# Optimization experiments

Hardware: AMD Instinct MI355X
Metric: run time of the kernel (lower is better)

Reference implementation:

```python
import jax, jax.numpy as jnp
import numpy as np

TARGET_SIZE = 1024
SOURCE_SIZE = 1024


def setup_inputs() -> dict:
    key = jax.random.key(0)
    k1, k2, k3, k4 = jax.random.split(key, 4)
    B, T, S = 16, 1024, 1024
    sentence_state = jax.random.normal(k1, (B, T, TARGET_SIZE), dtype=jnp.float32)
    graph_state = jax.random.normal(k2, (B, S, SOURCE_SIZE), dtype=jnp.float32)
    mask = jax.random.bernoulli(k3, 0.5, (B, T, S))  # bool
    # nn.Linear(target_size+source_size, 1, bias=False).weight flattened
    w = jax.random.normal(k4, (TARGET_SIZE + SOURCE_SIZE,), dtype=jnp.float32) * (
        1.0 / np.sqrt(TARGET_SIZE + SOURCE_SIZE)
    )
    return {"sentence_state": sentence_state, "graph_state": graph_state, "mask": mask, "w": w}


def reference(sentence_state, graph_state, mask, w):
    # Linear on concat([tgt, src]) with out_features=1 decomposes into two dot products:
    # score[b,t,s] = sentence[b,t,:] @ w_t + graph[b,s,:] @ w_s
    w_t = w[:TARGET_SIZE]
    w_s = w[TARGET_SIZE:]
    st = jnp.einsum("btd,d->bt", sentence_state, w_t)  # (B, T)
    gs = jnp.einsum("bsd,d->bs", graph_state, w_s)  # (B, S)
    scores = st[:, :, None] + gs[:, None, :]  # (B, T, S)
    attn = jax.nn.softmax(scores, axis=-1)
    attn = attn * (~mask).astype(attn.dtype)
    norm = jnp.sum(attn, axis=-1, keepdims=True) + 1e-12
    return attn / norm
```

## Files before the change

### kernel.cpp

```cpp
#include <hip/hip_runtime.h>


constexpr int Bb = 16;
constexpr int Tt = 1024;
constexpr int Ss = 1024;
constexpr int Dd = 1024;

__global__ void mask_probe_kernel(const unsigned char* __restrict__ m,
                                  int* __restrict__ ws_flag) {
  __shared__ int nz[4];
  const int t = threadIdx.x;
  if (t < 4) nz[t] = 0;
  __syncthreads();
  uchar4 v = reinterpret_cast<const uchar4*>(m)[t];
  if (v.x) atomicOr(&nz[0], 1);
  if (v.y) atomicOr(&nz[1], 1);
  if (v.z) atomicOr(&nz[2], 1);
  if (v.w) atomicOr(&nz[3], 1);
  __syncthreads();
  if (t == 0) {
    int spread = (nz[0] != 0) + (nz[1] != 0) + (nz[2] != 0) + (nz[3] != 0);
    ws_flag[0] = (spread >= 3) ? 0 : 1;
  }
}

__global__ __launch_bounds__(256) void gs_dot_kernel(
    const float* __restrict__ graph, const float* __restrict__ w_full,
    float* __restrict__ gs) {
  const int lane = threadIdx.x & 63;
  const int wv   = threadIdx.x >> 6;
  const long row = (long)blockIdx.x * 4 + wv;
  const float4* r  = reinterpret_cast<const float4*>(graph) + row * (Dd / 4);
  const float4* ws = reinterpret_cast<const float4*>(w_full + 1024);
  float acc = 0.f;
#pragma unroll
  for (int k = 0; k < 4; ++k) {
    float4 a = r[lane + 64 * k];
    float4 b = ws[lane + 64 * k];
    acc = fmaf(a.x, b.x, acc);
    acc = fmaf(a.y, b.y, acc);
    acc = fmaf(a.z, b.z, acc);
    acc = fmaf(a.w, b.w, acc);
  }
#pragma unroll
  for (int off = 32; off; off >>= 1) acc += __shfl_xor(acc, off, 64);
  if (lane == 0) gs[row] = acc;
}

__global__ __launch_bounds__(256) void PointerGenerator_9259949490200_kernel(
    const float* __restrict__ gs, const unsigned char* __restrict__ mask,
    const int* __restrict__ ws_flag, float* __restrict__ out) {
  __shared__ float p_sh[Ss];
  __shared__ float redbuf[8];
  const int tid  = threadIdx.x;
  const int lane = tid & 63;
  const int wv   = tid >> 6;
  const int b    = blockIdx.y;

  float4 g = reinterpret_cast<const float4*>(gs + (long)b * Ss)[tid];
  float m = fmaxf(fmaxf(g.x, g.y), fmaxf(g.z, g.w));
#pragma unroll
  for (int off = 32; off; off >>= 1) m = fmaxf(m, __shfl_xor(m, off, 64));
  if (lane == 0) redbuf[wv] = m;
  __syncthreads();
  m = fmaxf(fmaxf(redbuf[0], redbuf[1]), fmaxf(redbuf[2], redbuf[3]));
  float4 e = make_float4(__expf(g.x - m), __expf(g.y - m),
                         __expf(g.z - m), __expf(g.w - m));
  float zs = e.x + e.y + e.z + e.w;
#pragma unroll
  for (int off = 32; off; off >>= 1) zs += __shfl_xor(zs, off, 64);
  if (lane == 0) redbuf[4 + wv] = zs;
  __syncthreads();
  const float Z    = redbuf[4] + redbuf[5] + redbuf[6] + redbuf[7];
  const float invZ = 1.0f / Z;
  reinterpret_cast<float4*>(p_sh)[tid] =
      make_float4(e.x * invZ, e.y * invZ, e.z * invZ, e.w * invZ);
  __syncthreads();

  const long t    = (long)blockIdx.x * 4 + wv;
  const long row  = (long)b * Tt + t;
  const int  mode = ws_flag[0];

  uchar4 mk[4];
  if (mode == 0) {
    const uchar4* mrow = reinterpret_cast<const uchar4*>(mask + row * Ss);
#pragma unroll
    for (int k = 0; k < 4; ++k) mk[k] = mrow[lane + 64 * k];
  } else {
    const int4* mrow =
        reinterpret_cast<const int4*>(reinterpret_cast<const int*>(mask) + row * Ss);
#pragma unroll
    for (int k = 0; k < 4; ++k) {
      int4 w = mrow[lane + 64 * k];
      mk[k] = make_uchar4((unsigned char)(w.x != 0), (unsigned char)(w.y != 0),
                          (unsigned char)(w.z != 0), (unsigned char)(w.w != 0));
    }
  }

  float4 p[4];
  float sum = 0.f;
#pragma unroll
  for (int k = 0; k < 4; ++k) {
    const int idx = lane + 64 * k;
    p[k] = reinterpret_cast<const float4*>(p_sh)[idx];
    sum += (mk[k].x ? 0.f : p[k].x) + (mk[k].y ? 0.f : p[k].y) +
           (mk[k].z ? 0.f : p[k].z) + (mk[k].w ? 0.f : p[k].w);
  }
#pragma unroll
  for (int off = 32; off; off >>= 1) sum += __shfl_xor(sum, off, 64);
  const float invD = 1.0f / (sum + 1e-12f);
  float4* orow = reinterpret_cast<float4*>(out + row * Ss);
#pragma unroll
  for (int k = 0; k < 4; ++k) {
    const int idx = lane + 64 * k;
    float4 v;
    v.x = mk[k].x ? 0.f : p[k].x * invD;
    v.y = mk[k].y ? 0.f : p[k].y * invD;
    v.z = mk[k].z ? 0.f : p[k].z * invD;
    v.w = mk[k].w ? 0.f : p[k].w * invD;
    orow[idx] = v;
  }
}

extern "C" void kernel_launch(void* const* d_in, const int* in_sizes, int n_in,
                              void* d_out, int out_size, void* d_ws, size_t ws_size,
                              hipStream_t stream) {
  const float* graph        = (const float*)d_in[1];
  const unsigned char* mask = (const unsigned char*)d_in[2];
  const float* w            = (const float*)d_in[3];
  float* out = (float*)d_out;

  int*   ws_flag = (int*)d_ws;
  float* gs      = (float*)((char*)d_ws + 256);

  mask_probe_kernel<<<1, 256, 0, stream>>>(mask, ws_flag);
  gs_dot_kernel<<<(Bb * Ss) / 4, 256, 0, stream>>>(graph, w, gs);
  PointerGenerator_9259949490200_kernel<<<dim3(Tt / 4, Bb), 256, 0, stream>>>(
      gs, mask, ws_flag, out);
}
```

Measured before the change: 42.40 us.

## Precompute per-batch softmax once, process four rows per wave, nontemporal stores

Moves the per-batch softmax over gs out of the main kernel into a separate 16-block kernel that writes normalized probabilities to workspace and also performs the mask-format probe. The main kernel then loads those probabilities once per wave into registers and reuses them across four output rows, cutting the redundant softmax recomputation that every block previously did. Output writes use nontemporal stores to avoid polluting cache. The cost is an extra global round-trip for p, a serial extra launch dependency, and higher register use from holding four rows of masks.

```diff
diff --git a/kernel.cpp b/kernel.cpp
--- a/kernel.cpp
+++ b/kernel.cpp
@@ -6,23 +6,7 @@
 constexpr int Ss = 1024;
 constexpr int Dd = 1024;
 
-__global__ void mask_probe_kernel(const unsigned char* __restrict__ m,
-                                  int* __restrict__ ws_flag) {
-  __shared__ int nz[4];
-  const int t = threadIdx.x;
-  if (t < 4) nz[t] = 0;
-  __syncthreads();
-  uchar4 v = reinterpret_cast<const uchar4*>(m)[t];
-  if (v.x) atomicOr(&nz[0], 1);
-  if (v.y) atomicOr(&nz[1], 1);
-  if (v.z) atomicOr(&nz[2], 1);
-  if (v.w) atomicOr(&nz[3], 1);
-  __syncthreads();
-  if (t == 0) {
-    int spread = (nz[0] != 0) + (nz[1] != 0) + (nz[2] != 0) + (nz[3] != 0);
-    ws_flag[0] = (spread >= 3) ? 0 : 1;
-  }
-}
+typedef float f32x4 __attribute__((ext_vector_type(4)));
 
 __global__ __launch_bounds__(256) void gs_dot_kernel(
     const float* __restrict__ graph, const float* __restrict__ w_full,
@@ -47,15 +31,30 @@
   if (lane == 0) gs[row] = acc;
 }
 
-__global__ __launch_bounds__(256) void PointerGenerator_9259949490200_kernel(
+__global__ __launch_bounds__(256) void softmax_probe_kernel(
     const float* __restrict__ gs, const unsigned char* __restrict__ mask,
-    const int* __restrict__ ws_flag, float* __restrict__ out) {
-  __shared__ float p_sh[Ss];
+    int* __restrict__ ws_flag, float* __restrict__ p) {
   __shared__ float redbuf[8];
+  __shared__ int nz[4];
   const int tid  = threadIdx.x;
   const int lane = tid & 63;
   const int wv   = tid >> 6;
-  const int b    = blockIdx.y;
+  const int b    = blockIdx.x;
+
+  if (b == 0) {
+    if (tid < 4) nz[tid] = 0;
+    __syncthreads();
+    uchar4 v = reinterpret_cast<const uchar4*>(mask)[tid];
+    if (v.x) atomicOr(&nz[0], 1);
+    if (v.y) atomicOr(&nz[1], 1);
+    if (v.z) atomicOr(&nz[2], 1);
+    if (v.w) atomicOr(&nz[3], 1);
+    __syncthreads();
+    if (tid == 0) {
+      int spread = (nz[0] != 0) + (nz[1] != 0) + (nz[2] != 0) + (nz[3] != 0);
+      ws_flag[0] = (spread >= 3) ? 0 : 1;
+    }
+  }
 
   float4 g = reinterpret_cast<const float4*>(gs + (long)b * Ss)[tid];
   float m = fmaxf(fmaxf(g.x, g.y), fmaxf(g.z, g.w));
@@ -73,52 +72,76 @@
   __syncthreads();
   const float Z    = redbuf[4] + redbuf[5] + redbuf[6] + redbuf[7];
   const float invZ = 1.0f / Z;
-  reinterpret_cast<float4*>(p_sh)[tid] =
+  reinterpret_cast<float4*>(p + (long)b * Ss)[tid] =
       make_float4(e.x * invZ, e.y * invZ, e.z * invZ, e.w * invZ);
-  __syncthreads();
+}
 
-  const long t    = (long)blockIdx.x * 4 + wv;
-  const long row  = (long)b * Tt + t;
+__global__ __launch_bounds__(256) void PointerGenerator_9259949490200_kernel(
+    const float* __restrict__ p, const unsigned char* __restrict__ mask,
+    const int* __restrict__ ws_flag, float* __restrict__ out) {
+  constexpr int ROWS = 4;
+  const int lane = threadIdx.x & 63;
+  const int wv   = threadIdx.x >> 6;
+  const int b    = blockIdx.y;
+
+  const float4* p4 = reinterpret_cast<const float4*>(p + (long)b * Ss);
+  float4 pr[4];
+#pragma unroll
+  for (int k = 0; k < 4; ++k) pr[k] = p4[lane + 64 * k];
+
   const int  mode = ws_flag[0];
+  const long t0   = (long)blockIdx.x * (4 * ROWS) + (long)wv * ROWS;
+  const long row0 = (long)b * Tt + t0;
 
-  uchar4 mk[4];
+  uchar4 mk[ROWS][4];
   if (mode == 0) {
-    const uchar4* mrow = reinterpret_cast<const uchar4*>(mask + row * Ss);
+    const uchar4* m4 = reinterpret_cast<const uchar4*>(mask + row0 * Ss);
 #pragma unroll
-    for (int k = 0; k < 4; ++k) mk[k] = mrow[lane + 64 * k];
+    for (int r = 0; r < ROWS; ++r)
+#pragma unroll
+      for (int k = 0; k < 4; ++k) mk[r][k] = m4[r * 256 + lane + 64 * k];
   } else {
-    const int4* mrow =
-        reinterpret_cast<const int4*>(reinterpret_cast<const int*>(mask) + row * Ss);
+    const int4* m4 = reinterpret_cast<const int4*>(
+        reinterpret_cast<const int*>(mask) + row0 * Ss);
+#pragma unroll
+    for (int r = 0; r < ROWS; ++r)
+#pragma unroll
+      for (int k = 0; k < 4; ++k) {
+        int4 w = m4[r * 256 + lane + 64 * k];
+        mk[r][k] = make_uchar4((unsigned char)(w.x != 0), (unsigned char)(w.y != 0),
+                               (unsigned char)(w.z != 0), (unsigned char)(w.w != 0));
+      }
+  }
+
+  float sum[ROWS];
+#pragma unroll
+  for (int r = 0; r < ROWS; ++r) {
+    float s = 0.f;
 #pragma unroll
     for (int k = 0; k < 4; ++k) {
-      int4 w = mrow[lane + 64 * k];
-      mk[k] = make_uchar4((unsigned char)(w.x != 0), (unsigned char)(w.y != 0),
-                          (unsigned char)(w.z != 0), (unsigned char)(w.w != 0));
+      s += (mk[r][k].x ? 0.f : pr[k].x) + (mk[r][k].y ? 0.f : pr[k].y) +
+           (mk[r][k].z ? 0.f : pr[k].z) + (mk[r][k].w ? 0.f : pr[k].w);
     }
-  }
-
-  float4 p[4];
-  float sum = 0.f;
-#pragma unroll
-  for (int k = 0; k < 4; ++k) {
-    const int idx = lane + 64 * k;
-    p[k] = reinterpret_cast<const float4*>(p_sh)[idx];
-    sum += (mk[k].x ? 0.f : p[k].x) + (mk[k].y ? 0.f : p[k].y) +
-           (mk[k].z ? 0.f : p[k].z) + (mk[k].w ? 0.f : p[k].w);
+    sum[r] = s;
   }
 #pragma unroll
-  for (int off = 32; off; off >>= 1) sum += __shfl_xor(sum, off, 64);
-  const float invD = 1.0f / (sum + 1e-12f);
-  float4* orow = reinterpret_cast<float4*>(out + row * Ss);
+  for (int off = 32; off; off >>= 1)
 #pragma unroll
-  for (int k = 0; k < 4; ++k) {
-    const int idx = lane + 64 * k;
-    float4 v;
-    v.x = mk[k].x ? 0.f : p[k].x * invD;
-    v.y = mk[k].y ? 0.f : p[k].y * invD;
-    v.z = mk[k].z ? 0.f : p[k].z * invD;
-    v.w = mk[k].w ? 0.f : p[k].w * invD;
-    orow[idx] = v;
+    for (int r = 0; r < ROWS; ++r) sum[r] += __shfl_xor(sum[r], off, 64);
+
+#pragma unroll
+  for (int r = 0; r < ROWS; ++r) {
+    const float invD = 1.0f / (sum[r] + 1e-12f);
+    f32x4* orow = reinterpret_cast<f32x4*>(out + (row0 + r) * Ss);
+#pragma unroll
+    for (int k = 0; k < 4; ++k) {
+      f32x4 v;
+      v.x = mk[r][k].x ? 0.f : pr[k].x * invD;
+      v.y = mk[r][k].y ? 0.f : pr[k].y * invD;
+      v.z = mk[r][k].z ? 0.f : pr[k].z * invD;
+      v.w = mk[r][k].w ? 0.f : pr[k].w * invD;
+      __builtin_nontemporal_store(v, &orow[lane + 64 * k]);
+    }
   }
 }
 
@@ -132,9 +155,10 @@
 
   int*   ws_flag = (int*)d_ws;
   float* gs      = (float*)((char*)d_ws + 256);
+  float* p       = gs + Bb * Ss;
 
-  mask_probe_kernel<<<1, 256, 0, stream>>>(mask, ws_flag);
   gs_dot_kernel<<<(Bb * Ss) / 4, 256, 0, stream>>>(graph, w, gs);
-  PointerGenerator_9259949490200_kernel<<<dim3(Tt / 4, Bb), 256, 0, stream>>>(
-      gs, mask, ws_flag, out);
+  softmax_probe_kernel<<<Bb, 256, 0, stream>>>(gs, mask, ws_flag, p);
+  PointerGenerator_9259949490200_kernel<<<dim3(Tt / (4 * 4), Bb), 256, 0, stream>>>(
+      p, mask, ws_flag, out);
 }
```

New measurement: 38.44 us. 1.1x faster.
